# Kernel optimization log

Measured on AMD Instinct MI355X. Metric: run time of the kernel, lower is better.

The kernel has to match this reference:

```python
import jax, jax.numpy as jnp
import numpy as np
import math

EMBED = 1024
HEADS = 16
HEAD_DIM = EMBED // HEADS
B, S = 2, 2048


def setup_inputs() -> dict:
    key = jax.random.key(0)
    ks = jax.random.split(key, 12)
    sc = 1.0 / math.sqrt(EMBED)
    inp = {
        'query': jax.random.normal(ks[0], (B, S, EMBED), jnp.float32),
        'key': jax.random.normal(ks[1], (B, S, EMBED), jnp.float32),
        'values': jax.random.normal(ks[2], (B, S, EMBED), jnp.float32),
        # causal mask, broadcastable to [B, H, S, S]; masked where == 0
        'mask': jnp.tril(jnp.ones((S, S), jnp.int32))[None, None, :, :],
        'Wq': jax.random.normal(ks[3], (EMBED, EMBED), jnp.float32) * sc,
        'bq': jnp.zeros((EMBED,), jnp.float32),
        'Wk': jax.random.normal(ks[4], (EMBED, EMBED), jnp.float32) * sc,
        'bk': jnp.zeros((EMBED,), jnp.float32),
        'Wv': jax.random.normal(ks[5], (EMBED, EMBED), jnp.float32) * sc,
        'bv': jnp.zeros((EMBED,), jnp.float32),
        'Wo': jax.random.normal(ks[6], (EMBED, EMBED), jnp.float32) * sc,
        'bo': jnp.zeros((EMBED,), jnp.float32),
    }
    return inp


def reference(query, key, values, mask, Wq, bq, Wk, bk, Wv, bv, Wo, bo):
    # linear projections (torch Linear: x @ W.T + b)
    q = query @ Wq.T + bq
    k = key @ Wk.T + bk
    v = values @ Wv.T + bv
    b, sq, _ = q.shape
    sk = k.shape[1]
    q = q.reshape(b, sq, HEADS, HEAD_DIM)  # bqhd
    k = k.reshape(b, sk, HEADS, HEAD_DIM)  # bkhd
    v = v.reshape(b, sk, HEADS, HEAD_DIM)  # bkhd
    energy = jnp.einsum('bqhd,bkhd->bhqk', q, k) / math.sqrt(HEAD_DIM)
    energy = jnp.where(mask == 0, jnp.float32(-1e10), energy)
    attn = jax.nn.softmax(energy, axis=-1)
    out = jnp.einsum('bhqk,bkhd->bqhd', attn, v).reshape(b, sq, EMBED)
    return out @ Wo.T + bo
```

## Files before the change

kernel.cpp:

```cpp
#include <hip/hip_runtime.h>

typedef unsigned short u16;
typedef unsigned int   u32;
typedef __attribute__((ext_vector_type(4)))  float f32x4;
typedef __attribute__((ext_vector_type(8)))  short bf16x8;
typedef __attribute__((ext_vector_type(4)))  u32   u32x4;
typedef __attribute__((ext_vector_type(4)))  u16   u16x4;

#define AS1 __attribute__((address_space(1)))
#define AS3 __attribute__((address_space(3)))

__device__ __forceinline__ u16 f2bf(float f) {
  union { float f; u32 u; } v; v.f = f;
  u32 r = v.u + 0x7FFFu + ((v.u >> 16) & 1u);
  return (u16)(r >> 16);
}

__device__ __forceinline__ u16 f2bf_t(float f) {
  union { float f; u32 u; } v; v.f = f;
  return (u16)(v.u >> 16);
}

__device__ __forceinline__ void g2l16(const void* g, void* l) {
  __builtin_amdgcn_global_load_lds((const AS1 u32*)g, (AS3 u32*)l, 16, 0, 0);
}

struct CvtArgs {
  const float* src[7];
  u16*         dst[7];
  int          n4[7];
};

__global__ __launch_bounds__(256) void cvt_kernel(CvtArgs a) {
  const int ai = blockIdx.y;
  const f32x4* s = (const f32x4*)a.src[ai];
  u16x4*       d = (u16x4*)a.dst[ai];
  const int n4 = a.n4[ai];
  for (int i = blockIdx.x * 256 + threadIdx.x; i < n4; i += gridDim.x * 256) {
    f32x4 v = s[i];
    u16x4 o;
    o[0] = f2bf(v[0]); o[1] = f2bf(v[1]); o[2] = f2bf(v[2]); o[3] = f2bf(v[3]);
    d[i] = o;
  }
}

template <typename OutT, int TM>
__device__ __forceinline__ void gemm_core64(
    const u16* __restrict__ A, const u16* __restrict__ W,
    const float* __restrict__ bias, bool rowbias, float oscale,
    OutT* __restrict__ C, int ldc, int row0, int col0,
    u16* smem, int tid)
{
  constexpr int K = 1024;
  constexpr int MF = TM / 32;
  u16* sA = smem;
  u16* sB = smem + TM * 64;
  const int lane = tid & 63, wid = tid >> 6;
  const int l15 = lane & 15, hi = lane >> 4;
  const int wr = (wid >> 1) * (TM / 2), wc = (wid & 1) * 64;

  f32x4 acc[MF][4];
#pragma unroll
  for (int i = 0; i < MF; ++i)
#pragma unroll
    for (int j = 0; j < 4; ++j) acc[i][j] = f32x4{0.f, 0.f, 0.f, 0.f};

  auto stage = [&](int kt) {
#pragma unroll
    for (int it = 0; it < TM / 32; ++it) {
      int idx = it * 256 + tid;
      int r = idx >> 3, g = idx & 7;
      int gs = g ^ (r & 7);
      g2l16(A + (size_t)(row0 + r) * K + kt * 64 + gs * 8, sA + idx * 8);
    }
#pragma unroll
    for (int it = 0; it < 4; ++it) {
      int idx = it * 256 + tid;
      int r = idx >> 3, g = idx & 7;
      int gs = g ^ (r & 7);
      g2l16(W + (size_t)(col0 + r) * K + kt * 64 + gs * 8, sB + idx * 8);
    }
  };

  stage(0);
  for (int kt = 0; kt < K / 64; ++kt) {
    __syncthreads();
    bf16x8 aF[MF][2], bF[4][2];
#pragma unroll
    for (int mf = 0; mf < MF; ++mf) {
      int r = wr + mf * 16 + l15;
#pragma unroll
      for (int kh = 0; kh < 2; ++kh)
        aF[mf][kh] = *(const bf16x8*)(sA + r * 64 + ((kh * 4 + hi) ^ (r & 7)) * 8);
    }
#pragma unroll
    for (int nf = 0; nf < 4; ++nf) {
      int r = wc + nf * 16 + l15;
#pragma unroll
      for (int kh = 0; kh < 2; ++kh)
        bF[nf][kh] = *(const bf16x8*)(sB + r * 64 + ((kh * 4 + hi) ^ (r & 7)) * 8);
    }
    __syncthreads();
    if (kt + 1 < K / 64) stage(kt + 1);
#pragma unroll
    for (int kh = 0; kh < 2; ++kh)
#pragma unroll
      for (int mf = 0; mf < MF; ++mf)
#pragma unroll
        for (int nf = 0; nf < 4; ++nf)
          acc[mf][nf] = __builtin_amdgcn_mfma_f32_16x16x32_bf16(aF[mf][kh], bF[nf][kh], acc[mf][nf], 0, 0, 0);
  }

  if constexpr (sizeof(OutT) == 2) {
    constexpr int LDP = 136;
    u16* cL = smem;
#pragma unroll
    for (int nf = 0; nf < 4; ++nf) {
      int ccol = wc + nf * 16 + l15;
      float bcol = rowbias ? 0.f : bias[col0 + ccol];
#pragma unroll
      for (int mf = 0; mf < MF; ++mf) {
#pragma unroll
        for (int r = 0; r < 4; ++r) {
          int crow = wr + mf * 16 + hi * 4 + r;
          float bv = rowbias ? bias[row0 + crow] : bcol;
          cL[crow * LDP + ccol] = f2bf((acc[mf][nf][r] + bv) * oscale);
        }
      }
    }
    __syncthreads();
#pragma unroll
    for (int p = 0; p < TM / 16; ++p) {
      int idx = p * 256 + tid;
      int row = idx >> 4, ch = idx & 15;
      u32x4 w = *(const u32x4*)(cL + row * LDP + ch * 8);
      *(u32x4*)((u16*)C + (size_t)(row0 + row) * ldc + col0 + ch * 8) = w;
    }
  } else {
#pragma unroll
    for (int nf = 0; nf < 4; ++nf) {
      int gcol = col0 + wc + nf * 16 + l15;
      float bcol = rowbias ? 0.f : bias[gcol];
#pragma unroll
      for (int mf = 0; mf < MF; ++mf) {
#pragma unroll
        for (int r = 0; r < 4; ++r) {
          int grow = row0 + wr + mf * 16 + hi * 4 + r;
          float bv = rowbias ? bias[grow] : bcol;
          ((float*)C)[(size_t)grow * ldc + gcol] = (acc[mf][nf][r] + bv) * oscale;
        }
      }
    }
  }
}

struct ProjArgs {
  const u16* A[3]; const u16* W[3]; const float* bias[3];
  u16* C[3];
  float scale[3];
};

__global__ __launch_bounds__(256, 2) void gemm_proj(ProjArgs p) {
  __shared__ alignas(16) u16 smem[128 * 136];
  const int w = (blockIdx.x & 7) * 96 + (blockIdx.x >> 3);
  int which, row0, col0, ldc;
  bool rowbias;
  if (w < 512) {
    which = w >> 8;
    int l = w & 255;
    col0 = (l & 7) << 7;
    row0 = (l >> 3) << 7;
    ldc = 1024; rowbias = false;
  } else {
    which = 2;
    int l = w - 512;
    col0 = (l & 31) << 7;
    row0 = (l >> 5) << 7;
    ldc = 4096; rowbias = true;
  }
  gemm_core64<u16, 128>(p.A[which], p.W[which], p.bias[which], rowbias,
                        p.scale[which],
                        p.C[which], ldc, row0, col0, smem, threadIdx.x);
}

__global__ __launch_bounds__(256, 2) void gemm_out(
    const u16* __restrict__ A, const u16* __restrict__ W,
    const float* __restrict__ bias, float* __restrict__ C)
{
  __shared__ alignas(16) u16 smem[(64 + 128) * 64];
  const int w = (blockIdx.x & 7) * 64 + (blockIdx.x >> 3);
  const int col0 = (w & 7) << 7;
  const int row0 = (w >> 3) << 6;
  gemm_core64<float, 64>(A, W, bias, false, 1.0f, C, 1024, row0, col0,
                         smem, threadIdx.x);
}

__global__ __launch_bounds__(256, 4) void attn_fwd(
    const u16* __restrict__ Q, const u16* __restrict__ Kg, const u16* __restrict__ VT,
    u16* __restrict__ ctx)
{
  __shared__ alignas(16) u16 sK[2][64 * 64];
  __shared__ alignas(16) u16 sVt[2][64 * 64];
  __shared__ alignas(16) u16 sP[4][16 * 64];

  const int tid = threadIdx.x;
  const int lane = tid & 63, wid = tid >> 6;
  const int l15 = lane & 15, hi = lane >> 4;

  const int wg = blockIdx.x;
  const int jj = wg >> 5, bh = wg & 31;
  const int rr = jj >> 3, kk = jj & 7;
  int xt;
  if (rr == 0)      xt = 31 - kk;
  else if (rr == 1) xt = 16 + kk;
  else if (rr == 2) xt = 15 - kk;
  else              xt = kk;

  const int b = bh >> 4, h = bh & 15;
  const int q0 = xt * 64;
  const int q0w = q0 + wid * 16;
  const size_t base  = ((size_t)b * 2048) * 1024 + h * 64;
  const size_t vbase = (size_t)(h * 64) * 4096 + b * 2048;

  bf16x8 qf[2];
#pragma unroll
  for (int kh = 0; kh < 2; ++kh)
    qf[kh] = *(const bf16x8*)(Q + base + (size_t)(q0w + l15) * 1024 + kh * 32 + hi * 8);

  f32x4 o[4];
  float lS = 0.f;
#pragma unroll
  for (int nf = 0; nf < 4; ++nf) o[nf] = f32x4{0.f, 0.f, 0.f, 0.f};

  u16* sPw = &sP[wid][0];
  const int nt = xt + 1;

  auto issueK = [&](int ti, int bb) {
#pragma unroll
    for (int it = 0; it < 2; ++it) {
      int idx = it * 256 + tid;
      int r = idx >> 3, g = idx & 7;
      int gs = g ^ (r & 7);
      g2l16(Kg + base + (size_t)(ti * 64 + r) * 1024 + gs * 8, &sK[bb][idx * 8]);
    }
  };
  auto issueV = [&](int ti, int bb) {
#pragma unroll
    for (int it = 0; it < 2; ++it) {
      int idx = it * 256 + tid;
      int r = idx >> 3, g = idx & 7;
      int gs = g ^ (r & 7);
      g2l16(VT + vbase + (size_t)r * 4096 + ti * 64 + gs * 8, &sVt[bb][idx * 8]);
    }
  };

  issueK(0, 0);
  issueV(0, 0);
  __syncthreads();

  for (int ti = 0; ti < nt; ++ti) {
    const int cur = ti & 1;
    const bool pf = (ti + 1 < nt);
    if (pf) {
      issueK(ti + 1, cur ^ 1);
      issueV(ti + 1, cur ^ 1);
    }

    const int kv0 = ti * 64;
    const bool needmask = (ti == xt);
    const u16* sKc = &sK[cur][0];
    const u16* sVc = &sVt[cur][0];

    f32x4 s[4];
#pragma unroll
    for (int n = 0; n < 4; ++n) s[n] = f32x4{0.f, 0.f, 0.f, 0.f};
#pragma unroll
    for (int n = 0; n < 4; ++n) {
      int kvr = n * 16 + l15;
      bf16x8 kf0 = *(const bf16x8*)(sKc + kvr * 64 + ((hi) ^ (kvr & 7)) * 8);
      bf16x8 kf1 = *(const bf16x8*)(sKc + kvr * 64 + ((4 + hi) ^ (kvr & 7)) * 8);
      s[n] = __builtin_amdgcn_mfma_f32_16x16x32_bf16(kf0, qf[0], s[n], 0, 0, 0);
      s[n] = __builtin_amdgcn_mfma_f32_16x16x32_bf16(kf1, qf[1], s[n], 0, 0, 0);
    }

#pragma unroll
    for (int n = 0; n < 4; ++n) {
      int kabase = kv0 + n * 16 + hi * 4;
      int qa = q0w + l15;
#pragma unroll
      for (int r = 0; r < 4; ++r) {
        float sv = s[n][r];
        if (needmask && (kabase + r > qa)) sv = -1e30f;
        float p = __builtin_amdgcn_exp2f(sv);
        s[n][r] = p;
        lS += p;
      }
    }

#pragma unroll
    for (int n = 0; n < 4; ++n) {
      u16x4 pk;
      pk[0] = f2bf_t(s[n][0]); pk[1] = f2bf_t(s[n][1]);
      pk[2] = f2bf_t(s[n][2]); pk[3] = f2bf_t(s[n][3]);
      int kvb = n * 16 + hi * 4;
      *(u16x4*)(sPw + l15 * 64 + (kvb ^ ((l15 & 7) << 3))) = pk;
    }

#pragma unroll
    for (int kq = 0; kq < 2; ++kq) {
      bf16x8 pa, vb[4];
      pa = *(const bf16x8*)(sPw + l15 * 64 + ((kq * 32 + hi * 8) ^ ((l15 & 7) << 3)));
#pragma unroll
      for (int nf = 0; nf < 4; ++nf) {
        int rd = nf * 16 + l15;
        vb[nf] = *(const bf16x8*)(sVc + rd * 64 + ((kq * 4 + hi) ^ (rd & 7)) * 8);
      }
#pragma unroll
      for (int nf = 0; nf < 4; ++nf)
        o[nf] = __builtin_amdgcn_mfma_f32_16x16x32_bf16(pa, vb[nf], o[nf], 0, 0, 0);
    }

    __syncthreads();
  }

  float t = lS;
  t += __shfl_xor(t, 16);
  t += __shfl_xor(t, 32);
#pragma unroll
  for (int r = 0; r < 4; ++r) {
    float lr = __shfl(t, hi * 4 + r);
    float inv = 1.f / lr;
    size_t rowoff = base + (size_t)(q0w + hi * 4 + r) * 1024;
#pragma unroll
    for (int nf = 0; nf < 4; ++nf)
      ctx[rowoff + nf * 16 + l15] = f2bf(o[nf][r] * inv);
  }
}

extern "C" void kernel_launch(void* const* d_in, const int* in_sizes, int n_in,
                              void* d_out, int out_size, void* d_ws, size_t ws_size,
                              hipStream_t stream) {
  const float* query = (const float*)d_in[0];
  const float* key   = (const float*)d_in[1];
  const float* vals  = (const float*)d_in[2];
  const float* Wq = (const float*)d_in[4];
  const float* bq = (const float*)d_in[5];
  const float* Wk = (const float*)d_in[6];
  const float* bk = (const float*)d_in[7];
  const float* Wv = (const float*)d_in[8];
  const float* bv = (const float*)d_in[9];
  const float* Wo = (const float*)d_in[10];
  const float* bo = (const float*)d_in[11];
  float* out = (float*)d_out;

  if (ws_size < 58720256) return;

  u16* ws = (u16*)d_ws;
  u16* xq = ws + 0;
  u16* xk = ws + 4194304;
  u16* xv = ws + 8388608;
  u16* wq = ws + 12582912;
  u16* wk = ws + 13631488;
  u16* wv = ws + 14680064;
  u16* wo = ws + 15728640;
  u16* Qb = ws + 16777216;
  u16* Kb = ws + 20971520;
  u16* VT = ws + 25165824;
  u16* ctx = xq;

  CvtArgs ca;
  ca.src[0] = query; ca.dst[0] = xq; ca.n4[0] = 1048576;
  ca.src[1] = key;   ca.dst[1] = xk; ca.n4[1] = 1048576;
  ca.src[2] = vals;  ca.dst[2] = xv; ca.n4[2] = 1048576;
  ca.src[3] = Wq;    ca.dst[3] = wq; ca.n4[3] = 262144;
  ca.src[4] = Wk;    ca.dst[4] = wk; ca.n4[4] = 262144;
  ca.src[5] = Wv;    ca.dst[5] = wv; ca.n4[5] = 262144;
  ca.src[6] = Wo;    ca.dst[6] = wo; ca.n4[6] = 262144;
  cvt_kernel<<<dim3(256, 7), 256, 0, stream>>>(ca);

  constexpr float SCL = 0.125f * 1.44269504f;
  ProjArgs pa;
  pa.A[0] = xq; pa.W[0] = wq; pa.bias[0] = bq; pa.C[0] = Qb; pa.scale[0] = SCL;
  pa.A[1] = xk; pa.W[1] = wk; pa.bias[1] = bk; pa.C[1] = Kb; pa.scale[1] = 1.0f;
  pa.A[2] = wv; pa.W[2] = xv; pa.bias[2] = bv; pa.C[2] = VT; pa.scale[2] = 1.0f;
  gemm_proj<<<dim3(768), 256, 0, stream>>>(pa);

  attn_fwd<<<dim3(1024), 256, 0, stream>>>(Qb, Kb, VT, ctx);

  gemm_out<<<dim3(512), 256, 0, stream>>>(ctx, wo, bo, out);
}
```

Baseline: 103.9 us.

## Process 128 query rows per attention workgroup to reuse K/V tiles

The attention kernel now gives each workgroup 128 query rows, with 32 rows per wave split into two 16-row MFMA subtiles, instead of 64 rows. Each K/V tile loaded into LDS is therefore reused by twice as many queries, which halves global K/V traffic and LDS fragment reads per query. The grid drops from 1024 to 512 workgroups, launch bounds drop to 2 waves per EU, and each wave skips KV tiles lying entirely above its causal diagonal. The cost is fewer workgroups, more registers, and causal skipping that is coarser across waves inside a block, which can leave waves idle.

```diff
diff --git a/kernel.cpp b/kernel.cpp
--- a/kernel.cpp
+++ b/kernel.cpp
@@ -195,45 +195,40 @@
                          smem, threadIdx.x);
 }
 
-__global__ __launch_bounds__(256, 4) void attn_fwd(
+__global__ __launch_bounds__(256, 2) void attn_fwd(
     const u16* __restrict__ Q, const u16* __restrict__ Kg, const u16* __restrict__ VT,
     u16* __restrict__ ctx)
 {
   __shared__ alignas(16) u16 sK[2][64 * 64];
   __shared__ alignas(16) u16 sVt[2][64 * 64];
-  __shared__ alignas(16) u16 sP[4][16 * 64];
+  __shared__ alignas(16) u16 sP[4][32 * 64];
 
   const int tid = threadIdx.x;
   const int lane = tid & 63, wid = tid >> 6;
   const int l15 = lane & 15, hi = lane >> 4;
 
-  const int wg = blockIdx.x;
-  const int jj = wg >> 5, bh = wg & 31;
-  const int rr = jj >> 3, kk = jj & 7;
-  int xt;
-  if (rr == 0)      xt = 31 - kk;
-  else if (rr == 1) xt = 16 + kk;
-  else if (rr == 2) xt = 15 - kk;
-  else              xt = kk;
-
+  const int j = blockIdx.x >> 5, bh = blockIdx.x & 31;
+  const int X = (j < 8) ? (15 - j) : (j - 8);
   const int b = bh >> 4, h = bh & 15;
-  const int q0 = xt * 64;
-  const int q0w = q0 + wid * 16;
+  const int q0 = X * 128;
+  const int q0w = q0 + wid * 32;
   const size_t base  = ((size_t)b * 2048) * 1024 + h * 64;
   const size_t vbase = (size_t)(h * 64) * 4096 + b * 2048;
 
-  bf16x8 qf[2];
-#pragma unroll
-  for (int kh = 0; kh < 2; ++kh)
-    qf[kh] = *(const bf16x8*)(Q + base + (size_t)(q0w + l15) * 1024 + kh * 32 + hi * 8);
-
-  f32x4 o[4];
-  float lS = 0.f;
-#pragma unroll
-  for (int nf = 0; nf < 4; ++nf) o[nf] = f32x4{0.f, 0.f, 0.f, 0.f};
+  bf16x8 qfA[2], qfB[2];
+#pragma unroll
+  for (int kh = 0; kh < 2; ++kh) {
+    qfA[kh] = *(const bf16x8*)(Q + base + (size_t)(q0w + l15) * 1024 + kh * 32 + hi * 8);
+    qfB[kh] = *(const bf16x8*)(Q + base + (size_t)(q0w + 16 + l15) * 1024 + kh * 32 + hi * 8);
+  }
+
+  f32x4 oA[4], oB[4];
+  float lA = 0.f, lB = 0.f;
+#pragma unroll
+  for (int nf = 0; nf < 4; ++nf) { oA[nf] = f32x4{0.f, 0.f, 0.f, 0.f}; oB[nf] = f32x4{0.f, 0.f, 0.f, 0.f}; }
 
   u16* sPw = &sP[wid][0];
-  const int nt = xt + 1;
+  const int nt = 2 * X + 2;
 
   auto issueK = [&](int ti, int bb) {
 #pragma unroll
@@ -267,73 +262,105 @@
     }
 
     const int kv0 = ti * 64;
-    const bool needmask = (ti == xt);
+    const bool doit = (kv0 <= q0w + 31);
+    const bool needmask = (kv0 + 63 > q0w);
     const u16* sKc = &sK[cur][0];
     const u16* sVc = &sVt[cur][0];
 
-    f32x4 s[4];
-#pragma unroll
-    for (int n = 0; n < 4; ++n) s[n] = f32x4{0.f, 0.f, 0.f, 0.f};
-#pragma unroll
-    for (int n = 0; n < 4; ++n) {
-      int kvr = n * 16 + l15;
-      bf16x8 kf0 = *(const bf16x8*)(sKc + kvr * 64 + ((hi) ^ (kvr & 7)) * 8);
-      bf16x8 kf1 = *(const bf16x8*)(sKc + kvr * 64 + ((4 + hi) ^ (kvr & 7)) * 8);
-      s[n] = __builtin_amdgcn_mfma_f32_16x16x32_bf16(kf0, qf[0], s[n], 0, 0, 0);
-      s[n] = __builtin_amdgcn_mfma_f32_16x16x32_bf16(kf1, qf[1], s[n], 0, 0, 0);
-    }
-
-#pragma unroll
-    for (int n = 0; n < 4; ++n) {
-      int kabase = kv0 + n * 16 + hi * 4;
-      int qa = q0w + l15;
-#pragma unroll
-      for (int r = 0; r < 4; ++r) {
-        float sv = s[n][r];
-        if (needmask && (kabase + r > qa)) sv = -1e30f;
-        float p = __builtin_amdgcn_exp2f(sv);
-        s[n][r] = p;
-        lS += p;
-      }
-    }
-
-#pragma unroll
-    for (int n = 0; n < 4; ++n) {
-      u16x4 pk;
-      pk[0] = f2bf_t(s[n][0]); pk[1] = f2bf_t(s[n][1]);
-      pk[2] = f2bf_t(s[n][2]); pk[3] = f2bf_t(s[n][3]);
-      int kvb = n * 16 + hi * 4;
-      *(u16x4*)(sPw + l15 * 64 + (kvb ^ ((l15 & 7) << 3))) = pk;
-    }
-
-#pragma unroll
-    for (int kq = 0; kq < 2; ++kq) {
-      bf16x8 pa, vb[4];
-      pa = *(const bf16x8*)(sPw + l15 * 64 + ((kq * 32 + hi * 8) ^ ((l15 & 7) << 3)));
-#pragma unroll
-      for (int nf = 0; nf < 4; ++nf) {
-        int rd = nf * 16 + l15;
-        vb[nf] = *(const bf16x8*)(sVc + rd * 64 + ((kq * 4 + hi) ^ (rd & 7)) * 8);
-      }
-#pragma unroll
-      for (int nf = 0; nf < 4; ++nf)
-        o[nf] = __builtin_amdgcn_mfma_f32_16x16x32_bf16(pa, vb[nf], o[nf], 0, 0, 0);
+    if (doit) {
+      f32x4 sA_[4], sB_[4];
+#pragma unroll
+      for (int n = 0; n < 4; ++n) { sA_[n] = f32x4{0.f, 0.f, 0.f, 0.f}; sB_[n] = f32x4{0.f, 0.f, 0.f, 0.f}; }
+#pragma unroll
+      for (int n = 0; n < 4; ++n) {
+        int kvr = n * 16 + l15;
+        bf16x8 kf0 = *(const bf16x8*)(sKc + kvr * 64 + ((hi) ^ (kvr & 7)) * 8);
+        bf16x8 kf1 = *(const bf16x8*)(sKc + kvr * 64 + ((4 + hi) ^ (kvr & 7)) * 8);
+        sA_[n] = __builtin_amdgcn_mfma_f32_16x16x32_bf16(kf0, qfA[0], sA_[n], 0, 0, 0);
+        sA_[n] = __builtin_amdgcn_mfma_f32_16x16x32_bf16(kf1, qfA[1], sA_[n], 0, 0, 0);
+        sB_[n] = __builtin_amdgcn_mfma_f32_16x16x32_bf16(kf0, qfB[0], sB_[n], 0, 0, 0);
+        sB_[n] = __builtin_amdgcn_mfma_f32_16x16x32_bf16(kf1, qfB[1], sB_[n], 0, 0, 0);
+      }
+
+#pragma unroll
+      for (int n = 0; n < 4; ++n) {
+        int kabase = kv0 + n * 16 + hi * 4;
+        int qaA = q0w + l15;
+#pragma unroll
+        for (int r = 0; r < 4; ++r) {
+          float sv = sA_[n][r];
+          if (needmask && (kabase + r > qaA)) sv = -1e30f;
+          float p = __builtin_amdgcn_exp2f(sv);
+          sA_[n][r] = p;
+          lA += p;
+        }
+        u16x4 pk;
+        pk[0] = f2bf_t(sA_[n][0]); pk[1] = f2bf_t(sA_[n][1]);
+        pk[2] = f2bf_t(sA_[n][2]); pk[3] = f2bf_t(sA_[n][3]);
+        int kvb = n * 16 + hi * 4;
+        *(u16x4*)(sPw + l15 * 64 + (kvb ^ ((l15 & 7) << 3))) = pk;
+      }
+#pragma unroll
+      for (int n = 0; n < 4; ++n) {
+        int kabase = kv0 + n * 16 + hi * 4;
+        int qaB = q0w + 16 + l15;
+#pragma unroll
+        for (int r = 0; r < 4; ++r) {
+          float sv = sB_[n][r];
+          if (needmask && (kabase + r > qaB)) sv = -1e30f;
+          float p = __builtin_amdgcn_exp2f(sv);
+          sB_[n][r] = p;
+          lB += p;
+        }
+        u16x4 pk;
+        pk[0] = f2bf_t(sB_[n][0]); pk[1] = f2bf_t(sB_[n][1]);
+        pk[2] = f2bf_t(sB_[n][2]); pk[3] = f2bf_t(sB_[n][3]);
+        int kvb = n * 16 + hi * 4;
+        *(u16x4*)(sPw + (16 + l15) * 64 + (kvb ^ ((l15 & 7) << 3))) = pk;
+      }
+
+#pragma unroll
+      for (int kq = 0; kq < 2; ++kq) {
+        bf16x8 vb[4];
+#pragma unroll
+        for (int nf = 0; nf < 4; ++nf) {
+          int rd = nf * 16 + l15;
+          vb[nf] = *(const bf16x8*)(sVc + rd * 64 + ((kq * 4 + hi) ^ (rd & 7)) * 8);
+        }
+        bf16x8 paA = *(const bf16x8*)(sPw + l15 * 64 + ((kq * 32 + hi * 8) ^ ((l15 & 7) << 3)));
+        bf16x8 paB = *(const bf16x8*)(sPw + (16 + l15) * 64 + ((kq * 32 + hi * 8) ^ ((l15 & 7) << 3)));
+#pragma unroll
+        for (int nf = 0; nf < 4; ++nf) {
+          oA[nf] = __builtin_amdgcn_mfma_f32_16x16x32_bf16(paA, vb[nf], oA[nf], 0, 0, 0);
+          oB[nf] = __builtin_amdgcn_mfma_f32_16x16x32_bf16(paB, vb[nf], oB[nf], 0, 0, 0);
+        }
+      }
     }
 
     __syncthreads();
   }
 
-  float t = lS;
-  t += __shfl_xor(t, 16);
-  t += __shfl_xor(t, 32);
+  float tA = lA;
+  tA += __shfl_xor(tA, 16);
+  tA += __shfl_xor(tA, 32);
+  float tB = lB;
+  tB += __shfl_xor(tB, 16);
+  tB += __shfl_xor(tB, 32);
 #pragma unroll
   for (int r = 0; r < 4; ++r) {
-    float lr = __shfl(t, hi * 4 + r);
-    float inv = 1.f / lr;
-    size_t rowoff = base + (size_t)(q0w + hi * 4 + r) * 1024;
+    float lrA = __shfl(tA, hi * 4 + r);
+    float invA = 1.f / lrA;
+    size_t rowA = base + (size_t)(q0w + hi * 4 + r) * 1024;
 #pragma unroll
     for (int nf = 0; nf < 4; ++nf)
-      ctx[rowoff + nf * 16 + l15] = f2bf(o[nf][r] * inv);
+      ctx[rowA + nf * 16 + l15] = f2bf(oA[nf][r] * invA);
+
+    float lrB = __shfl(tB, hi * 4 + r);
+    float invB = 1.f / lrB;
+    size_t rowB = base + (size_t)(q0w + 16 + hi * 4 + r) * 1024;
+#pragma unroll
+    for (int nf = 0; nf < 4; ++nf)
+      ctx[rowB + nf * 16 + l15] = f2bf(oB[nf][r] * invB);
   }
 }
 
@@ -385,7 +412,7 @@
   pa.A[2] = wv; pa.W[2] = xv; pa.bias[2] = bv; pa.C[2] = VT; pa.scale[2] = 1.0f;
   gemm_proj<<<dim3(768), 256, 0, stream>>>(pa);
 
-  attn_fwd<<<dim3(1024), 256, 0, stream>>>(Qb, Kb, VT, ctx);
+  attn_fwd<<<dim3(512), 256, 0, stream>>>(Qb, Kb, VT, ctx);
 
   gemm_out<<<dim3(512), 256, 0, stream>>>(ctx, wo, bo, out);
 }
```

New measurement: 118.5 us. +14.1%, slower.
